# Optimization experiments

Hardware: AMD Instinct MI355X
Metric: run time of the kernel (lower is better)

The kernel has to match this reference:

```python
import jax, jax.numpy as jnp
import numpy as np

N_HEAD = 16
WINDOW = 256


def setup_inputs() -> dict:
    key = jax.random.key(0)
    ks = jax.random.split(key, 3)
    B, S, D = 2, 2048, 1024
    x = jax.random.normal(ks[0], (B, S, D), dtype=jnp.float32)
    w_attn = jax.random.normal(ks[1], (D, 3 * D), dtype=jnp.float32) * 0.02
    b_attn = jnp.zeros((3 * D,), dtype=jnp.float32)
    w_proj = jax.random.normal(ks[2], (D, D), dtype=jnp.float32) * 0.02
    b_proj = jnp.zeros((D,), dtype=jnp.float32)
    return {"x": x, "w_attn": w_attn, "b_attn": b_attn, "w_proj": w_proj, "b_proj": b_proj}


def reference(x, w_attn, b_attn, w_proj, b_proj):
    B, S, D = x.shape
    hd = D // N_HEAD  # head dim
    scale = 1.0 / np.sqrt(hd).astype(np.float32)

    # fused QKV projection (Conv1D == linear on last dim)
    c = jnp.einsum('bsd,df->bsf', x, w_attn) + b_attn
    q, k, v = jnp.split(c, 3, axis=-1)

    def split_heads(t):  # [B,S,D] -> [B,H,S,hd]
        return t.reshape(B, S, N_HEAD, hd).transpose(0, 2, 1, 3)

    q, k, v = split_heads(q), split_heads(k), split_heads(v)
    present = jnp.stack([k, v], axis=1)  # [B,2,H,S,hd]

    # scores [B,H,S,S]
    w = jnp.einsum('bhqd,bhkd->bhqk', q, k) * scale

    # causal sliding-window mask
    q_pos = jnp.arange(S)[:, None]
    k_pos = jnp.arange(S)[None, :]
    mask = (k_pos <= q_pos) & (k_pos >= q_pos - WINDOW + 1)  # [S,S]
    w = jnp.where(mask[None, None], w, jnp.finfo(w.dtype).min)
    w = jax.nn.softmax(w, axis=-1)

    a = jnp.einsum('bhqk,bhkd->bhqd', w, v)
    a = a.transpose(0, 2, 1, 3).reshape(B, S, D)  # merge heads
    out = jnp.einsum('bsd,df->bsf', a, w_proj) + b_proj
    return out, present
```

## Files before the change

kernel.cpp:

```cpp
#include <hip/hip_runtime.h>
#include <cstdint>
#include <cstddef>

typedef __bf16 bf16x8 __attribute__((ext_vector_type(8)));
typedef float f32x4 __attribute__((ext_vector_type(4)));

#define MFMA16(a, b, c) __builtin_amdgcn_mfma_f32_16x16x32_bf16(a, b, c, 0, 0, 0)

static __device__ __forceinline__ bf16x8 ld_bf16x8(const __bf16* p) {
    return *reinterpret_cast<const bf16x8*>(p);
}

static __device__ __forceinline__ void async_cp16(const __bf16* g, __bf16* l) {
    __builtin_amdgcn_global_load_lds((const __attribute__((address_space(1))) void*)g,
                                     (__attribute__((address_space(3))) void*)l, 16, 0, 0);
}

template <int N>
static __device__ __forceinline__ void wait_vmcnt() {
    asm volatile("s_waitcnt vmcnt(%0)" ::"n"(N) : "memory");
}

static __device__ __forceinline__ void barrier_pinned() {
    __builtin_amdgcn_sched_barrier(0);
    __builtin_amdgcn_s_barrier();
    __builtin_amdgcn_sched_barrier(0);
}

static __device__ __forceinline__ float ex2(float x) {
    return __builtin_amdgcn_exp2f(x);
}

template <int CTRL>
static __device__ __forceinline__ float dppmv(float x) {
    return __builtin_bit_cast(float, __builtin_amdgcn_update_dpp(
        0, __builtin_bit_cast(int, x), CTRL, 0xF, 0xF, true));
}
static __device__ __forceinline__ float rmax16(float x) {
    x = fmaxf(x, dppmv<0x121>(x));
    x = fmaxf(x, dppmv<0x122>(x));
    x = fmaxf(x, dppmv<0x124>(x));
    x = fmaxf(x, dppmv<0x128>(x));
    return x;
}
static __device__ __forceinline__ float rsum16(float x) {
    x += dppmv<0x121>(x);
    x += dppmv<0x122>(x);
    x += dppmv<0x124>(x);
    x += dppmv<0x128>(x);
    return x;
}

__global__ void cvt_kernel(const float* __restrict__ src, __bf16* __restrict__ dst, int n8) {
    int i = blockIdx.x * blockDim.x + threadIdx.x;
    if (i >= n8) return;
    const float4* s4 = reinterpret_cast<const float4*>(src) + (size_t)i * 2;
    float4 a = s4[0], b = s4[1];
    bf16x8 o;
    o[0] = (__bf16)a.x; o[1] = (__bf16)a.y; o[2] = (__bf16)a.z; o[3] = (__bf16)a.w;
    o[4] = (__bf16)b.x; o[5] = (__bf16)b.y; o[6] = (__bf16)b.z; o[7] = (__bf16)b.w;
    reinterpret_cast<bf16x8*>(dst)[i] = o;
}

__global__ __launch_bounds__(256) void tcvt_kernel(const float* __restrict__ in,
                                                   __bf16* __restrict__ out, int K, int N) {
    __shared__ __bf16 T[64][72];
    const int k0 = blockIdx.y * 64, n0 = blockIdx.x * 64;
    const int t = threadIdx.x;
    const int col = (t & 15) << 2;
    const int rowb = t >> 4;
    #pragma unroll
    for (int i = 0; i < 4; i++) {
        int row = i * 16 + rowb;
        float4 v = *reinterpret_cast<const float4*>(&in[(size_t)(k0 + row) * N + n0 + col]);
        T[col + 0][row] = (__bf16)v.x;
        T[col + 1][row] = (__bf16)v.y;
        T[col + 2][row] = (__bf16)v.z;
        T[col + 3][row] = (__bf16)v.w;
    }
    __syncthreads();
    const int oc = (t & 7) << 3;
    const int orb = t >> 3;
    #pragma unroll
    for (int i = 0; i < 2; i++) {
        int r = i * 32 + orb;
        bf16x8 v = *reinterpret_cast<bf16x8*>(&T[r][oc]);
        *reinterpret_cast<bf16x8*>(&out[(size_t)(n0 + r) * K + k0 + oc]) = v;
    }
}

template <int BM, int BN, int WM, int WN>
__device__ __forceinline__ void mainloop2(const __bf16* __restrict__ A,
                                          const __bf16* __restrict__ Bt,
                                          int K, int row0, int col0,
                                          __bf16* lds,
                                          f32x4 (&acc)[BM / WM / 16][BN / WN / 16]) {
    constexpr int MR = BM / WM / 16, NR = BN / WN / 16;
    constexpr int AE = BM * 32;
    constexpr int BUFE = AE + BN * 32;
    constexpr int APW = BM / 16 / 8;
    constexpr int BPW = BN / 16 / 8;
    const int tid = threadIdx.x, l = tid & 63, w = tid >> 6;
    const int wm = w / WN, wn = w % WN;
    const int lr = l >> 2;
    const int lcs = (((l & 3) ^ ((l >> 3) & 3)) << 3);
    const int fr = l & 15;
    const int fc = (((l >> 4) ^ ((l >> 1) & 3)) << 3);

    const size_t arow = (size_t)(row0 + lr) * K + lcs;
    const size_t brow = (size_t)(col0 + lr) * K + lcs;
    const int nt = K >> 5;

    auto stage = [&](int t, int buf) {
        const int k0 = t << 5;
        const int bb = buf * BUFE;
        #pragma unroll
        for (int j = 0; j < APW; j++) {
            const int mi = w * APW + j;
            async_cp16(A + arow + (size_t)mi * 16 * K + k0, lds + bb + mi * 512 + l * 8);
        }
        #pragma unroll
        for (int j = 0; j < BPW; j++) {
            const int ni = w * BPW + j;
            async_cp16(Bt + brow + (size_t)ni * 16 * K + k0, lds + bb + AE + ni * 512 + l * 8);
        }
    };

    stage(0, 0);
    stage(1, 1);

    const int aoff = (wm * (BM / WM) + fr) * 32 + fc;
    const int boff = AE + (wn * (BN / WN) + fr) * 32 + fc;

    int p = 0;
    for (int t = 0; t < nt; ++t) {
        if (t + 1 < nt) {
            wait_vmcnt<APW + BPW>();
        } else {
            wait_vmcnt<0>();
        }
        barrier_pinned();
        if (t + 2 < nt) {
            int p2 = p + 2; if (p2 >= 3) p2 -= 3;
            stage(t + 2, p2);
        }
        const int cb = p * BUFE;
        bf16x8 af[MR], bfv[NR];
        #pragma unroll
        for (int m = 0; m < MR; m++) af[m] = ld_bf16x8(&lds[cb + aoff + m * 512]);
        #pragma unroll
        for (int n = 0; n < NR; n++) bfv[n] = ld_bf16x8(&lds[cb + boff + n * 512]);
        __builtin_amdgcn_s_setprio(1);
        #pragma unroll
        for (int m = 0; m < MR; m++) {
            #pragma unroll
            for (int n = 0; n < NR; n++) {
                acc[m][n] = MFMA16(af[m], bfv[n], acc[m][n]);
            }
        }
        __builtin_amdgcn_s_setprio(0);
        asm volatile("s_waitcnt lgkmcnt(0)" ::: "memory");
        __builtin_amdgcn_sched_barrier(0);
        p = (p == 2) ? 0 : p + 1;
    }
}

__global__ __launch_bounds__(512, 2) void gemm_qkv_kernel(const __bf16* __restrict__ xb,
                                                          const __bf16* __restrict__ wabt,
                                                          const float* __restrict__ bias,
                                                          __bf16* __restrict__ qb,
                                                          __bf16* __restrict__ kb,
                                                          __bf16* __restrict__ vt,
                                                          float* __restrict__ present) {
    __shared__ __bf16 lds[3 * (128 * 32 + 128 * 32)];
    f32x4 acc[2][4] = {};
    const int row0 = blockIdx.y * 128, col0 = blockIdx.x * 128;
    mainloop2<128, 128, 4, 2>(xb, wabt, 1024, row0, col0, lds, acc);

    const int l = threadIdx.x & 63, w = threadIdx.x >> 6;
    const int wm = w >> 1, wn = w & 1;
    const int part = col0 >> 10;
    #pragma unroll
    for (int n = 0; n < 4; n++) {
        int col = col0 + wn * 64 + n * 16 + (l & 15);
        int hh = (col >> 6) & 15;
        int dd = col & 63;
        float bv = bias[col];
        #pragma unroll
        for (int m = 0; m < 2; m++) {
            #pragma unroll
            for (int r = 0; r < 4; r++) {
                int row = row0 + wm * 32 + m * 16 + ((l >> 4) << 2) + r;
                int bb = row >> 11, ss = row & 2047;
                float val = acc[m][n][r] + bv;
                size_t qi = (((size_t)(bb * 16 + hh)) * 2048 + ss) * 64 + dd;
                if (part == 0) {
                    qb[qi] = (__bf16)val;
                } else if (part == 1) {
                    kb[qi] = (__bf16)val;
                    present[(((size_t)((bb * 2 + 0) * 16 + hh)) * 2048 + ss) * 64 + dd] = val;
                } else {
                    vt[(((size_t)(bb * 16 + hh)) * 64 + dd) * 2048 + ss] = (__bf16)val;
                    present[(((size_t)((bb * 2 + 1) * 16 + hh)) * 2048 + ss) * 64 + dd] = val;
                }
            }
        }
    }
}

__global__ __launch_bounds__(512, 2) void gemm_proj_kernel(const __bf16* __restrict__ ab,
                                                           const __bf16* __restrict__ wpbt,
                                                           const float* __restrict__ bias,
                                                           float* __restrict__ out) {
    __shared__ __bf16 lds[3 * (128 * 32 + 128 * 32)];
    f32x4 acc[2][4] = {};
    const int row0 = blockIdx.y * 128, col0 = blockIdx.x * 128;
    mainloop2<128, 128, 4, 2>(ab, wpbt, 1024, row0, col0, lds, acc);

    const int lane = threadIdx.x & 63, w = threadIdx.x >> 6;
    const int wm = w >> 1, wn = w & 1;
    #pragma unroll
    for (int n = 0; n < 4; n++) {
        int col = col0 + wn * 64 + n * 16 + (lane & 15);
        float bv = bias[col];
        #pragma unroll
        for (int m = 0; m < 2; m++) {
            #pragma unroll
            for (int r = 0; r < 4; r++) {
                int row = row0 + wm * 32 + m * 16 + ((lane >> 4) << 2) + r;
                out[(size_t)row * 1024 + col] = acc[m][n][r] + bv;
            }
        }
    }
}

__global__ __launch_bounds__(256) void attn_kernel(const __bf16* __restrict__ qb,
                                                   const __bf16* __restrict__ kb,
                                                   const __bf16* __restrict__ vtb,
                                                   __bf16* __restrict__ ab) {
    __shared__ __bf16 Pls[4][16 * 72];
    __shared__ float combsh[2176];
    const int bidx = blockIdx.x;
    const int xcd = bidx & 7, idx = bidx >> 3;
    const int bh = (xcd << 2) | (idx & 3);
    const int qt = idx >> 2;
    const int lane = threadIdx.x & 63, wid = threadIdx.x >> 6;
    const int qsub = wid >> 1, half = wid & 1;
    const int q0w = qt * 32 + qsub * 16;

    const __bf16* Qh = qb + (size_t)bh * 2048 * 64;
    const __bf16* Kh = kb + (size_t)bh * 2048 * 64;
    const __bf16* Vt = vtb + (size_t)bh * 64 * 2048;
    __bf16* Pw = &Pls[wid][0];

    const int ld16 = lane & 15, hi3 = (lane >> 4) << 3, hi4 = (lane >> 4) << 2;

    bf16x8 qf[2];
    {
        const __bf16* qp = Qh + (size_t)(q0w + ld16) * 64 + hi3;
        qf[0] = ld_bf16x8(qp);
        qf[1] = ld_bf16x8(qp + 32);
    }

    f32x4 o[4];
    #pragma unroll
    for (int dt = 0; dt < 4; dt++) o[dt] = (f32x4){0.f, 0.f, 0.f, 0.f};
    float mrun[4] = {-1e30f, -1e30f, -1e30f, -1e30f};
    float srun[4] = {0.f, 0.f, 0.f, 0.f};

    const float cl2 = 0.18033688f;
    int klo = q0w - 255;
    int kt0 = klo > 0 ? (klo & ~63) : 0;
    const int ktend = q0w + 15;

    for (int kt = kt0 + half * 64; kt <= ktend; kt += 128) {
        bf16x8 kf[4][2];
        #pragma unroll
        for (int kc = 0; kc < 4; kc++) {
            const __bf16* kp = Kh + (size_t)(kt + kc * 16 + ld16) * 64 + hi3;
            kf[kc][0] = ld_bf16x8(kp);
            kf[kc][1] = ld_bf16x8(kp + 32);
        }
        bf16x8 va[4], vb[4];
        #pragma unroll
        for (int dt = 0; dt < 4; dt++) {
            const __bf16* vp = &Vt[(size_t)(dt * 16 + ld16) * 2048 + kt + hi3];
            va[dt] = ld_bf16x8(vp);
            vb[dt] = ld_bf16x8(vp + 32);
        }
        f32x4 s[4];
        __builtin_amdgcn_s_setprio(1);
        #pragma unroll
        for (int kc = 0; kc < 4; kc++) {
            f32x4 a = (f32x4){0.f, 0.f, 0.f, 0.f};
            a = MFMA16(qf[0], kf[kc][0], a);
            a = MFMA16(qf[1], kf[kc][1], a);
            s[kc] = a;
        }
        __builtin_amdgcn_s_setprio(0);
        const bool clean = (kt >= q0w - 240) && (kt + 63 <= q0w);
        float pv0[4], pv1[4], pv2[4], pv3[4];
        if (clean) {
            float mxs[4];
            #pragma unroll
            for (int r = 0; r < 4; r++) {
                float m = fmaxf(fmaxf(s[0][r], s[1][r]), fmaxf(s[2][r], s[3][r]));
                mxs[r] = rmax16(m) * cl2;
            }
            float grow = fmaxf(fmaxf(mxs[0] - mrun[0], mxs[1] - mrun[1]),
                               fmaxf(mxs[2] - mrun[2], mxs[3] - mrun[3]));
            if (__all(grow <= 8.f)) {
                #pragma unroll
                for (int r = 0; r < 4; r++) {
                    float p0 = ex2(s[0][r] * cl2 - mrun[r]);
                    float p1 = ex2(s[1][r] * cl2 - mrun[r]);
                    float p2 = ex2(s[2][r] * cl2 - mrun[r]);
                    float p3 = ex2(s[3][r] * cl2 - mrun[r]);
                    srun[r] += rsum16((p0 + p1) + (p2 + p3));
                    pv0[r] = p0; pv1[r] = p1; pv2[r] = p2; pv3[r] = p3;
                }
            } else {
                float factor[4];
                #pragma unroll
                for (int r = 0; r < 4; r++) {
                    float mn = fmaxf(mrun[r], mxs[r]);
                    float f = ex2(mrun[r] - mn);
                    float p0 = ex2(s[0][r] * cl2 - mn);
                    float p1 = ex2(s[1][r] * cl2 - mn);
                    float p2 = ex2(s[2][r] * cl2 - mn);
                    float p3 = ex2(s[3][r] * cl2 - mn);
                    srun[r] = srun[r] * f + rsum16((p0 + p1) + (p2 + p3));
                    mrun[r] = mn;
                    factor[r] = f;
                    pv0[r] = p0; pv1[r] = p1; pv2[r] = p2; pv3[r] = p3;
                }
                #pragma unroll
                for (int dt = 0; dt < 4; dt++) {
                    #pragma unroll
                    for (int r = 0; r < 4; r++) o[dt][r] *= factor[r];
                }
            }
        } else {
            float factor[4];
            #pragma unroll
            for (int r = 0; r < 4; r++) {
                int q = q0w + hi4 + r;
                int kb0 = kt + ld16;
                bool ok0 = (kb0 <= q) && (kb0 > q - 256);
                bool ok1 = (kb0 + 16 <= q) && (kb0 + 16 > q - 256);
                bool ok2 = (kb0 + 32 <= q) && (kb0 + 32 > q - 256);
                bool ok3 = (kb0 + 48 <= q) && (kb0 + 48 > q - 256);
                float t0 = ok0 ? s[0][r] * cl2 : -1e30f;
                float t1 = ok1 ? s[1][r] * cl2 : -1e30f;
                float t2 = ok2 ? s[2][r] * cl2 : -1e30f;
                float t3 = ok3 ? s[3][r] * cl2 : -1e30f;
                float mx = rmax16(fmaxf(fmaxf(t0, t1), fmaxf(t2, t3)));
                float mn = fmaxf(mrun[r], mx);
                float f = ex2(mrun[r] - mn);
                float p0 = ok0 ? ex2(t0 - mn) : 0.f;
                float p1 = ok1 ? ex2(t1 - mn) : 0.f;
                float p2 = ok2 ? ex2(t2 - mn) : 0.f;
                float p3 = ok3 ? ex2(t3 - mn) : 0.f;
                srun[r] = srun[r] * f + rsum16((p0 + p1) + (p2 + p3));
                mrun[r] = mn;
                factor[r] = f;
                pv0[r] = p0; pv1[r] = p1; pv2[r] = p2; pv3[r] = p3;
            }
            #pragma unroll
            for (int dt = 0; dt < 4; dt++) {
                #pragma unroll
                for (int r = 0; r < 4; r++) o[dt][r] *= factor[r];
            }
        }
        #pragma unroll
        for (int r = 0; r < 4; r++) {
            int qrow = hi4 + r;
            Pw[qrow * 72 + ld16]      = (__bf16)pv0[r];
            Pw[qrow * 72 + 16 + ld16] = (__bf16)pv1[r];
            Pw[qrow * 72 + 32 + ld16] = (__bf16)pv2[r];
            Pw[qrow * 72 + 48 + ld16] = (__bf16)pv3[r];
        }
        asm volatile("s_waitcnt lgkmcnt(0)" ::: "memory");
        bf16x8 pfA = ld_bf16x8(&Pw[ld16 * 72 + hi3]);
        bf16x8 pfB = ld_bf16x8(&Pw[ld16 * 72 + 32 + hi3]);
        __builtin_amdgcn_s_setprio(1);
        #pragma unroll
        for (int dt = 0; dt < 4; dt++) o[dt] = MFMA16(pfA, va[dt], o[dt]);
        #pragma unroll
        for (int dt = 0; dt < 4; dt++) o[dt] = MFMA16(pfB, vb[dt], o[dt]);
        __builtin_amdgcn_s_setprio(0);
    }

    if (half == 1) {
        #pragma unroll
        for (int dt = 0; dt < 4; dt++) {
            #pragma unroll
            for (int r = 0; r < 4; r++) {
                combsh[(qsub * 16 + hi4 + r) * 66 + dt * 16 + ld16] = o[dt][r];
            }
        }
        if (ld16 == 0) {
            #pragma unroll
            for (int r = 0; r < 4; r++) {
                combsh[2112 + qsub * 16 + hi4 + r] = mrun[r];
                combsh[2144 + qsub * 16 + hi4 + r] = srun[r];
            }
        }
    }
    __syncthreads();
    if (half == 0) {
        float f0[4], f1[4];
        #pragma unroll
        for (int r = 0; r < 4; r++) {
            float m1 = combsh[2112 + qsub * 16 + hi4 + r];
            float s1 = combsh[2144 + qsub * 16 + hi4 + r];
            float mm = fmaxf(mrun[r], m1);
            f0[r] = ex2(mrun[r] - mm);
            f1[r] = ex2(m1 - mm);
            srun[r] = srun[r] * f0[r] + s1 * f1[r];
        }
        const int bb = bh >> 4, hh = bh & 15;
        #pragma unroll
        for (int r = 0; r < 4; r++) {
            int q = q0w + hi4 + r;
            float inv = 1.f / srun[r];
            size_t base = ((size_t)bb * 2048 + q) * 1024 + hh * 64;
            #pragma unroll
            for (int dt = 0; dt < 4; dt++) {
                float o1 = combsh[(qsub * 16 + hi4 + r) * 66 + dt * 16 + ld16];
                ab[base + dt * 16 + ld16] = (__bf16)((o[dt][r] * f0[r] + o1 * f1[r]) * inv);
            }
        }
    }
}

extern "C" void kernel_launch(void* const* d_in, const int* in_sizes, int n_in,
                              void* d_out, int out_size, void* d_ws, size_t ws_size,
                              hipStream_t stream) {
    const float* x = (const float*)d_in[0];
    const float* w_attn = (const float*)d_in[1];
    const float* b_attn = (const float*)d_in[2];
    const float* w_proj = (const float*)d_in[3];
    const float* b_proj = (const float*)d_in[4];

    float* out = (float*)d_out;
    float* present = out + (size_t)2 * 2048 * 1024;

    char* w = (char*)d_ws;
    __bf16* xb   = (__bf16*)(w);
    __bf16* wabt = (__bf16*)(w + 8388608);
    __bf16* wpbt = (__bf16*)(w + 14680064);
    __bf16* qb   = (__bf16*)(w + 16777216);
    __bf16* kb   = (__bf16*)(w + 25165824);
    __bf16* vt   = (__bf16*)(w + 33554432);
    __bf16* ab   = xb;

    cvt_kernel<<<2048, 256, 0, stream>>>(x, xb, 524288);
    tcvt_kernel<<<dim3(48, 16), 256, 0, stream>>>(w_attn, wabt, 1024, 3072);
    tcvt_kernel<<<dim3(16, 16), 256, 0, stream>>>(w_proj, wpbt, 1024, 1024);

    gemm_qkv_kernel<<<dim3(24, 32), 512, 0, stream>>>(xb, wabt, b_attn, qb, kb, vt, present);

    attn_kernel<<<2048, 256, 0, stream>>>(qb, kb, vt, ab);

    gemm_proj_kernel<<<dim3(8, 32), 512, 0, stream>>>(ab, wpbt, b_proj, out);
}
```

Measured before the change: 120.0 us.

## Replace online softmax loop with fully unrolled three-tile exact softmax

```diff
diff --git a/kernel.cpp b/kernel.cpp
--- a/kernel.cpp
+++ b/kernel.cpp
@@ -238,7 +238,7 @@
                                                    const __bf16* __restrict__ kb,
                                                    const __bf16* __restrict__ vtb,
                                                    __bf16* __restrict__ ab) {
-    __shared__ __bf16 Pls[4][16 * 72];
+    __shared__ __bf16 Pls[4][2][16 * 72];
     __shared__ float combsh[2176];
     const int bidx = blockIdx.x;
     const int xcd = bidx & 7, idx = bidx >> 3;
@@ -251,7 +251,6 @@
     const __bf16* Qh = qb + (size_t)bh * 2048 * 64;
     const __bf16* Kh = kb + (size_t)bh * 2048 * 64;
     const __bf16* Vt = vtb + (size_t)bh * 64 * 2048;
-    __bf16* Pw = &Pls[wid][0];
 
     const int ld16 = lane & 15, hi3 = (lane >> 4) << 3, hi4 = (lane >> 4) << 2;
 
@@ -262,125 +261,117 @@
         qf[1] = ld_bf16x8(qp + 32);
     }
 
-    f32x4 o[4];
-    #pragma unroll
-    for (int dt = 0; dt < 4; dt++) o[dt] = (f32x4){0.f, 0.f, 0.f, 0.f};
-    float mrun[4] = {-1e30f, -1e30f, -1e30f, -1e30f};
-    float srun[4] = {0.f, 0.f, 0.f, 0.f};
-
     const float cl2 = 0.18033688f;
     int klo = q0w - 255;
     int kt0 = klo > 0 ? (klo & ~63) : 0;
     const int ktend = q0w + 15;
-
-    for (int kt = kt0 + half * 64; kt <= ktend; kt += 128) {
-        bf16x8 kf[4][2];
+    const int ktA = kt0 + half * 64;
+    const int ktB = ktA + 128;
+    const int ktC = ktA + 256;
+    const bool actA = ktA <= ktend, actB = ktB <= ktend, actC = ktC <= ktend;
+
+    auto qk = [&](int kt, f32x4 (&s)[4]) {
         #pragma unroll
         for (int kc = 0; kc < 4; kc++) {
             const __bf16* kp = Kh + (size_t)(kt + kc * 16 + ld16) * 64 + hi3;
-            kf[kc][0] = ld_bf16x8(kp);
-            kf[kc][1] = ld_bf16x8(kp + 32);
-        }
-        bf16x8 va[4], vb[4];
+            bf16x8 k0 = ld_bf16x8(kp);
+            bf16x8 k1 = ld_bf16x8(kp + 32);
+            f32x4 a = (f32x4){0.f, 0.f, 0.f, 0.f};
+            a = MFMA16(qf[0], k0, a);
+            a = MFMA16(qf[1], k1, a);
+            s[kc] = a;
+        }
+        const bool clean = (kt >= q0w - 240) && (kt + 63 <= q0w);
+        if (!clean) {
+            #pragma unroll
+            for (int r = 0; r < 4; r++) {
+                int q = q0w + hi4 + r;
+                #pragma unroll
+                for (int kc = 0; kc < 4; kc++) {
+                    int ki = kt + kc * 16 + ld16;
+                    bool ok = (ki <= q) && (ki > q - 256);
+                    s[kc][r] = ok ? s[kc][r] : -1e30f;
+                }
+            }
+        }
+    };
+    auto ldV = [&](int kt, bf16x8 (&va)[4], bf16x8 (&vb)[4]) {
         #pragma unroll
         for (int dt = 0; dt < 4; dt++) {
             const __bf16* vp = &Vt[(size_t)(dt * 16 + ld16) * 2048 + kt + hi3];
             va[dt] = ld_bf16x8(vp);
             vb[dt] = ld_bf16x8(vp + 32);
         }
-        f32x4 s[4];
-        __builtin_amdgcn_s_setprio(1);
-        #pragma unroll
-        for (int kc = 0; kc < 4; kc++) {
-            f32x4 a = (f32x4){0.f, 0.f, 0.f, 0.f};
-            a = MFMA16(qf[0], kf[kc][0], a);
-            a = MFMA16(qf[1], kf[kc][1], a);
-            s[kc] = a;
-        }
-        __builtin_amdgcn_s_setprio(0);
-        const bool clean = (kt >= q0w - 240) && (kt + 63 <= q0w);
-        float pv0[4], pv1[4], pv2[4], pv3[4];
-        if (clean) {
-            float mxs[4];
-            #pragma unroll
-            for (int r = 0; r < 4; r++) {
-                float m = fmaxf(fmaxf(s[0][r], s[1][r]), fmaxf(s[2][r], s[3][r]));
-                mxs[r] = rmax16(m) * cl2;
-            }
-            float grow = fmaxf(fmaxf(mxs[0] - mrun[0], mxs[1] - mrun[1]),
-                               fmaxf(mxs[2] - mrun[2], mxs[3] - mrun[3]));
-            if (__all(grow <= 8.f)) {
-                #pragma unroll
-                for (int r = 0; r < 4; r++) {
-                    float p0 = ex2(s[0][r] * cl2 - mrun[r]);
-                    float p1 = ex2(s[1][r] * cl2 - mrun[r]);
-                    float p2 = ex2(s[2][r] * cl2 - mrun[r]);
-                    float p3 = ex2(s[3][r] * cl2 - mrun[r]);
-                    srun[r] += rsum16((p0 + p1) + (p2 + p3));
-                    pv0[r] = p0; pv1[r] = p1; pv2[r] = p2; pv3[r] = p3;
-                }
-            } else {
-                float factor[4];
-                #pragma unroll
-                for (int r = 0; r < 4; r++) {
-                    float mn = fmaxf(mrun[r], mxs[r]);
-                    float f = ex2(mrun[r] - mn);
-                    float p0 = ex2(s[0][r] * cl2 - mn);
-                    float p1 = ex2(s[1][r] * cl2 - mn);
-                    float p2 = ex2(s[2][r] * cl2 - mn);
-                    float p3 = ex2(s[3][r] * cl2 - mn);
-                    srun[r] = srun[r] * f + rsum16((p0 + p1) + (p2 + p3));
-                    mrun[r] = mn;
-                    factor[r] = f;
-                    pv0[r] = p0; pv1[r] = p1; pv2[r] = p2; pv3[r] = p3;
-                }
-                #pragma unroll
-                for (int dt = 0; dt < 4; dt++) {
-                    #pragma unroll
-                    for (int r = 0; r < 4; r++) o[dt][r] *= factor[r];
-                }
-            }
-        } else {
-            float factor[4];
-            #pragma unroll
-            for (int r = 0; r < 4; r++) {
-                int q = q0w + hi4 + r;
-                int kb0 = kt + ld16;
-                bool ok0 = (kb0 <= q) && (kb0 > q - 256);
-                bool ok1 = (kb0 + 16 <= q) && (kb0 + 16 > q - 256);
-                bool ok2 = (kb0 + 32 <= q) && (kb0 + 32 > q - 256);
-                bool ok3 = (kb0 + 48 <= q) && (kb0 + 48 > q - 256);
-                float t0 = ok0 ? s[0][r] * cl2 : -1e30f;
-                float t1 = ok1 ? s[1][r] * cl2 : -1e30f;
-                float t2 = ok2 ? s[2][r] * cl2 : -1e30f;
-                float t3 = ok3 ? s[3][r] * cl2 : -1e30f;
-                float mx = rmax16(fmaxf(fmaxf(t0, t1), fmaxf(t2, t3)));
-                float mn = fmaxf(mrun[r], mx);
-                float f = ex2(mrun[r] - mn);
-                float p0 = ok0 ? ex2(t0 - mn) : 0.f;
-                float p1 = ok1 ? ex2(t1 - mn) : 0.f;
-                float p2 = ok2 ? ex2(t2 - mn) : 0.f;
-                float p3 = ok3 ? ex2(t3 - mn) : 0.f;
-                srun[r] = srun[r] * f + rsum16((p0 + p1) + (p2 + p3));
-                mrun[r] = mn;
-                factor[r] = f;
-                pv0[r] = p0; pv1[r] = p1; pv2[r] = p2; pv3[r] = p3;
-            }
-            #pragma unroll
-            for (int dt = 0; dt < 4; dt++) {
-                #pragma unroll
-                for (int r = 0; r < 4; r++) o[dt][r] *= factor[r];
-            }
-        }
+    };
+
+    f32x4 sA[4], sB[4], sC[4];
+    #pragma unroll
+    for (int kc = 0; kc < 4; kc++) {
+        sA[kc] = (f32x4){-1e30f, -1e30f, -1e30f, -1e30f};
+        sB[kc] = (f32x4){-1e30f, -1e30f, -1e30f, -1e30f};
+        sC[kc] = (f32x4){-1e30f, -1e30f, -1e30f, -1e30f};
+    }
+    bf16x8 vaA[4], vbA[4], vaB[4], vbB[4], vaC[4], vbC[4];
+    if (actA) qk(ktA, sA);
+    if (actA) ldV(ktA, vaA, vbA);
+    if (actB) qk(ktB, sB);
+    if (actC) qk(ktC, sC);
+
+    float mrun[4], srun[4];
+    if (actA) {
+        #pragma unroll
+        for (int r = 0; r < 4; r++) {
+            float m = fmaxf(fmaxf(sA[0][r], sA[1][r]), fmaxf(sA[2][r], sA[3][r]));
+            m = fmaxf(m, fmaxf(fmaxf(sB[0][r], sB[1][r]), fmaxf(sB[2][r], sB[3][r])));
+            m = fmaxf(m, fmaxf(fmaxf(sC[0][r], sC[1][r]), fmaxf(sC[2][r], sC[3][r])));
+            mrun[r] = rmax16(m) * cl2;
+        }
+        #pragma unroll
+        for (int r = 0; r < 4; r++) {
+            float acc = 0.f;
+            #pragma unroll
+            for (int kc = 0; kc < 4; kc++) {
+                float p = ex2(fmaf(sA[kc][r], cl2, -mrun[r]));
+                sA[kc][r] = p;
+                acc += p;
+            }
+            #pragma unroll
+            for (int kc = 0; kc < 4; kc++) {
+                float p = ex2(fmaf(sB[kc][r], cl2, -mrun[r]));
+                sB[kc][r] = p;
+                acc += p;
+            }
+            #pragma unroll
+            for (int kc = 0; kc < 4; kc++) {
+                float p = ex2(fmaf(sC[kc][r], cl2, -mrun[r]));
+                sC[kc][r] = p;
+                acc += p;
+            }
+            srun[r] = rsum16(acc);
+        }
+    } else {
+        #pragma unroll
+        for (int r = 0; r < 4; r++) {
+            mrun[r] = -1e30f;
+            srun[r] = 0.f;
+        }
+    }
+
+    f32x4 o[4];
+    #pragma unroll
+    for (int dt = 0; dt < 4; dt++) o[dt] = (f32x4){0.f, 0.f, 0.f, 0.f};
+
+    auto wrP = [&](__bf16* Pw, f32x4 (&s)[4]) {
         #pragma unroll
         for (int r = 0; r < 4; r++) {
             int qrow = hi4 + r;
-            Pw[qrow * 72 + ld16]      = (__bf16)pv0[r];
-            Pw[qrow * 72 + 16 + ld16] = (__bf16)pv1[r];
-            Pw[qrow * 72 + 32 + ld16] = (__bf16)pv2[r];
-            Pw[qrow * 72 + 48 + ld16] = (__bf16)pv3[r];
-        }
-        asm volatile("s_waitcnt lgkmcnt(0)" ::: "memory");
+            Pw[qrow * 72 + ld16]      = (__bf16)s[0][r];
+            Pw[qrow * 72 + 16 + ld16] = (__bf16)s[1][r];
+            Pw[qrow * 72 + 32 + ld16] = (__bf16)s[2][r];
+            Pw[qrow * 72 + 48 + ld16] = (__bf16)s[3][r];
+        }
+    };
+    auto pv = [&](__bf16* Pw, bf16x8 (&va)[4], bf16x8 (&vb)[4]) {
         bf16x8 pfA = ld_bf16x8(&Pw[ld16 * 72 + hi3]);
         bf16x8 pfB = ld_bf16x8(&Pw[ld16 * 72 + 32 + hi3]);
         __builtin_amdgcn_s_setprio(1);
@@ -389,6 +380,26 @@
         #pragma unroll
         for (int dt = 0; dt < 4; dt++) o[dt] = MFMA16(pfB, vb[dt], o[dt]);
         __builtin_amdgcn_s_setprio(0);
+    };
+
+    __bf16* Pw0 = &Pls[wid][0][0];
+    __bf16* Pw1 = &Pls[wid][1][0];
+    if (actA) {
+        wrP(Pw0, sA);
+        if (actB) ldV(ktB, vaB, vbB);
+        asm volatile("s_waitcnt lgkmcnt(0)" ::: "memory");
+        pv(Pw0, vaA, vbA);
+    }
+    if (actB) {
+        wrP(Pw1, sB);
+        if (actC) ldV(ktC, vaC, vbC);
+        asm volatile("s_waitcnt lgkmcnt(0)" ::: "memory");
+        pv(Pw1, vaB, vbB);
+    }
+    if (actC) {
+        wrP(Pw0, sC);
+        asm volatile("s_waitcnt lgkmcnt(0)" ::: "memory");
+        pv(Pw0, vaC, vbC);
     }
 
     if (half == 1) {
```

Result: no change. 120.9 us (+0.8%).
